# Kernel optimization log

Hardware: AMD Instinct MI355X
Metric: run time of the kernel (lower is better)

Reference implementation:

```python
import jax, jax.numpy as jnp
import numpy as np

B, T, D = 1024, 20, 50          # batch sessions, seq len (hardcoded 20), emb dim (hardcoded 50)
S1S2 = 50 * 20                  # sample1 * sample2 friend nodes (GAT src)
DEG = 50                        # avg in-degree per dst node
E = B * DEG
NUM_USERS, NUM_ITEMS = 100000, 50000


def _lstm(x, W_ih, W_hh, b_ih, b_hh):
    """PyTorch-style LSTM (gate order i,f,g,o). x: [N,T,D] -> hs: [T,N,D]."""
    N = x.shape[0]
    h0 = jnp.zeros((N, x.shape[-1]), x.dtype)
    def step(carry, xt):
        h, c = carry
        gates = xt @ W_ih.T + h @ W_hh.T + b_ih + b_hh
        i, f, g, o = jnp.split(gates, 4, axis=-1)
        c = jax.nn.sigmoid(f) * c + jax.nn.sigmoid(i) * jnp.tanh(g)
        h = jax.nn.sigmoid(o) * jnp.tanh(c)
        return (h, c), h
    (_, _), hs = jax.lax.scan(step, (h0, h0), jnp.swapaxes(x, 0, 1))
    return hs


def _gat(feat_src, feat_dst, edge_src, edge_dst, fc_W, fc_b):
    """u_dot_v -> edge_softmax (per dst) -> u_mul_e_sum -> relu(fc)."""
    n_dst = feat_dst.shape[0]
    src_e = feat_src[edge_src]                           # [E, D] gather
    score = jnp.sum(src_e * feat_dst[edge_dst], axis=-1) # [E] u_dot_v
    m = jax.ops.segment_max(score, edge_dst, num_segments=n_dst)
    ex = jnp.exp(score - m[edge_dst])
    den = jax.ops.segment_sum(ex, edge_dst, num_segments=n_dst)
    w = ex / den[edge_dst]                               # edge_softmax
    agg = jax.ops.segment_sum(w[:, None] * src_e, edge_dst, num_segments=n_dst)
    return jax.nn.relu(agg @ fc_W.T + fc_b)


def setup_inputs() -> dict:
    key = jax.random.key(0)
    ks = jax.random.split(key, 16)
    input_session = jax.random.randint(ks[0], (B, T), 0, NUM_ITEMS, dtype=jnp.int32)
    support_nodes_layer1 = jax.random.randint(ks[1], (S1S2,), 0, NUM_USERS, dtype=jnp.int32)
    support_sessions_layer1 = jax.random.randint(ks[2], (S1S2, T), 0, NUM_ITEMS, dtype=jnp.int32)
    edge_src = jax.random.randint(ks[3], (E,), 0, S1S2, dtype=jnp.int32)
    edge_dst = jnp.repeat(jnp.arange(B, dtype=jnp.int32), DEG)  # every dst has DEG edges
    s = 0.05
    user_emb = jax.random.normal(ks[4], (NUM_USERS, D), jnp.float32) * s
    item_emb = (jax.random.normal(ks[5], (NUM_ITEMS, D), jnp.float32) * s).at[0].set(0.0)  # padding_idx=0
    W_ih = jax.random.normal(ks[6], (4 * D, D), jnp.float32) * s
    W_hh = jax.random.normal(ks[7], (4 * D, D), jnp.float32) * s
    b_ih = jax.random.normal(ks[8], (4 * D,), jnp.float32) * s
    b_hh = jax.random.normal(ks[9], (4 * D,), jnp.float32) * s
    W1 = jax.random.normal(ks[10], (D, 2 * D), jnp.float32) * s
    fc_W = jax.random.normal(ks[11], (D, D), jnp.float32) * s
    fc_b = jax.random.normal(ks[12], (D,), jnp.float32) * s
    W2 = jax.random.normal(ks[13], (D, 3 * D), jnp.float32) * s
    return {"input_session": input_session, "support_nodes_layer1": support_nodes_layer1,
            "support_sessions_layer1": support_sessions_layer1, "edge_src": edge_src,
            "edge_dst": edge_dst, "user_emb": user_emb, "item_emb": item_emb,
            "W_ih": W_ih, "W_hh": W_hh, "b_ih": b_ih, "b_hh": b_hh,
            "W1": W1, "fc_W": fc_W, "fc_b": fc_b, "W2": W2}


def reference(input_session, support_nodes_layer1, support_sessions_layer1, edge_src, edge_dst,
              user_emb, item_emb, W_ih, W_hh, b_ih, b_hh, W1, fc_W, fc_b, W2):
    # current-user short-term: LSTM over session item embeddings, take last hidden
    output = _lstm(item_emb[input_session], W_ih, W_hh, b_ih, b_hh)[-1]        # [B, D]
    # friends long-term (user emb) + short-term (LSTM over friend sessions, step 0 as in source)
    long_term1 = user_emb[support_nodes_layer1]                                 # [S1S2, D]
    short_term1 = _lstm(item_emb[support_sessions_layer1], W_ih, W_hh, b_ih, b_hh)[0]  # [S1S2, D]
    ls1 = jax.nn.relu(jnp.concatenate([long_term1, short_term1], axis=-1) @ W1.T)      # [S1S2, D]
    # GAT: gather -> per-dst edge softmax -> scatter weighted sum
    gat_out = _gat(ls1, output, edge_src, edge_dst, fc_W, fc_b)                 # [B, D]
    feat = jnp.concatenate([output, gat_out], axis=-1)                          # [B, 2D]
    sr = jnp.concatenate([output, feat], axis=-1) @ W2.T                        # [B, D]
    logits = sr @ item_emb[1:].T                                                # [B, NUM_ITEMS-1]
    return logits
```

## Files before the change

kernel.cpp:

```cpp
#include <hip/hip_runtime.h>
#include <math.h>

#define D 50
#define T 20
#define BATCH 1024
#define S1S2 1000
#define DEG 50
#define NITEMS 50000
#define NLOGITS 49999
#define KPAD 64
#define NIPAD 50048
#define LROW 520

using bf16x8 = __attribute__((ext_vector_type(8))) __bf16;
using f32x4  = __attribute__((ext_vector_type(4))) float;

__device__ __forceinline__ float sigf(float x) { return 1.0f / (1.0f + expf(-x)); }

__device__ __forceinline__ unsigned short f2bf(float f) {
    unsigned u = __builtin_bit_cast(unsigned, f);
    u = (u + 0x7FFFu + ((u >> 16) & 1u)) >> 16;
    return (unsigned short)u;
}

__global__ __launch_bounds__(256) void lstm_main_kernel(
    const int* __restrict__ sess,
    const float* __restrict__ item_emb,
    const float* __restrict__ W_ih,
    const float* __restrict__ W_hh,
    const float* __restrict__ b_ih,
    const float* __restrict__ b_hh,
    float* __restrict__ out_h)
{
    const int b = blockIdx.x;
    const int t = threadIdx.x;
    __shared__ float x_s[D];
    __shared__ float h_s[D];
    __shared__ float g_s[4 * D];
    __shared__ int idx_s[T];

    if (t < T) idx_s[t] = sess[b * T + t];

    float wih[D], whh[D];
    float bias = 0.f;
    if (t < 4 * D) {
        #pragma unroll
        for (int k = 0; k < D; ++k) {
            wih[k] = W_ih[t * D + k];
            whh[k] = W_hh[t * D + k];
        }
        bias = b_ih[t] + b_hh[t];
    }
    float c = 0.f;
    if (t < D) h_s[t] = 0.f;
    __syncthreads();

    for (int step = 0; step < T; ++step) {
        if (t < D) x_s[t] = item_emb[(size_t)idx_s[step] * D + t];
        __syncthreads();
        if (t < 4 * D) {
            float g = bias;
            #pragma unroll
            for (int k = 0; k < D; ++k)
                g += wih[k] * x_s[k] + whh[k] * h_s[k];
            g_s[t] = g;
        }
        __syncthreads();
        if (t < D) {
            float ig = sigf(g_s[t]);
            float fg = sigf(g_s[D + t]);
            float gg = tanhf(g_s[2 * D + t]);
            float og = sigf(g_s[3 * D + t]);
            c = fg * c + ig * gg;
            h_s[t] = og * tanhf(c);
        }
        __syncthreads();
    }
    if (t < D) out_h[b * D + t] = h_s[t];
}

__global__ __launch_bounds__(256) void friends_kernel(
    const int* __restrict__ nodes,
    const int* __restrict__ fsess,
    const float* __restrict__ user_emb,
    const float* __restrict__ item_emb,
    const float* __restrict__ W_ih,
    const float* __restrict__ W_hh,
    const float* __restrict__ b_ih,
    const float* __restrict__ b_hh,
    const float* __restrict__ W1,
    float* __restrict__ ls1)
{
    const int s = blockIdx.x;
    const int t = threadIdx.x;
    __shared__ float x_s[D];
    __shared__ float h_s[D];
    __shared__ float g_s[4 * D];

    if (t < D) x_s[t] = item_emb[(size_t)fsess[s * T] * D + t];
    __syncthreads();
    if (t < 4 * D) {
        float g = b_ih[t] + b_hh[t];
        #pragma unroll
        for (int k = 0; k < D; ++k) g += W_ih[t * D + k] * x_s[k];
        g_s[t] = g;
    }
    __syncthreads();
    if (t < D) {
        float ig = sigf(g_s[t]);
        float gg = tanhf(g_s[2 * D + t]);
        float og = sigf(g_s[3 * D + t]);
        float c1 = ig * gg;
        h_s[t] = og * tanhf(c1);
    }
    __syncthreads();
    if (t < D) {
        const int node = nodes[s];
        const float* ue = user_emb + (size_t)node * D;
        const float* w1r = W1 + t * 2 * D;
        float acc = 0.f;
        #pragma unroll
        for (int k = 0; k < D; ++k) acc += ue[k] * w1r[k];
        #pragma unroll
        for (int k = 0; k < D; ++k) acc += h_s[k] * w1r[D + k];
        ls1[s * D + t] = fmaxf(acc, 0.f);
    }
}

__global__ __launch_bounds__(64) void gat_sr_kernel(
    const float* __restrict__ out_h,
    const float* __restrict__ ls1,
    const int* __restrict__ edge_src,
    const float* __restrict__ fc_W,
    const float* __restrict__ fc_b,
    const float* __restrict__ W2,
    unsigned* __restrict__ sr_u)
{
    const int b = blockIdx.x;
    const int l = threadIdx.x;
    __shared__ float q[D];
    __shared__ int srcs[DEG];
    __shared__ float w_s[DEG];
    __shared__ float a_s[D];
    __shared__ float g_s[D];
    __shared__ float srow_s[KPAD];

    srow_s[l] = 0.f;
    if (l < D) q[l] = out_h[b * D + l];
    if (l < DEG) srcs[l] = edge_src[b * DEG + l];
    __syncthreads();

    float sc = -INFINITY;
    if (l < DEG) {
        const float* row = ls1 + (size_t)srcs[l] * D;
        float s = 0.f;
        #pragma unroll
        for (int k = 0; k < D; ++k) s += row[k] * q[k];
        sc = s;
    }
    float m = sc;
    #pragma unroll
    for (int off = 32; off; off >>= 1) m = fmaxf(m, __shfl_xor(m, off));
    float ex = (l < DEG) ? expf(sc - m) : 0.f;
    float den = ex;
    #pragma unroll
    for (int off = 32; off; off >>= 1) den += __shfl_xor(den, off);
    if (l < DEG) w_s[l] = ex / den;
    __syncthreads();

    if (l < D) {
        float a = 0.f;
        #pragma unroll
        for (int j = 0; j < DEG; ++j) a += w_s[j] * ls1[(size_t)srcs[j] * D + l];
        a_s[l] = a;
    }
    __syncthreads();
    if (l < D) {
        float g = fc_b[l];
        #pragma unroll
        for (int k = 0; k < D; ++k) g += a_s[k] * fc_W[l * D + k];
        g_s[l] = fmaxf(g, 0.f);
    }
    __syncthreads();
    if (l < D) {
        const float* w2r = W2 + l * 3 * D;
        float v = 0.f;
        #pragma unroll
        for (int k = 0; k < D; ++k) v += q[k] * (w2r[k] + w2r[D + k]);
        #pragma unroll
        for (int k = 0; k < D; ++k) v += g_s[k] * w2r[2 * D + k];
        srow_s[l] = v;
    }
    __syncthreads();
    if (l < KPAD / 2) {
        unsigned u = (unsigned)f2bf(srow_s[2 * l]) |
                     ((unsigned)f2bf(srow_s[2 * l + 1]) << 16);
        sr_u[b * (KPAD / 2) + l] = u;
    }
}

__global__ __launch_bounds__(256) void item_prep_kernel(
    const float* __restrict__ item_emb,
    unsigned* __restrict__ item_u)
{
    const int idx = blockIdx.x * 256 + threadIdx.x;
    if (idx >= NIPAD * (KPAD / 2)) return;
    const int r = idx >> 5, c2 = idx & 31;
    const int c0 = c2 * 2, c1 = c0 + 1;
    float f0 = 0.f, f1 = 0.f;
    if (r < NLOGITS) {
        const float* row = item_emb + (size_t)(1 + r) * D;
        if (c0 < D) f0 = row[c0];
        if (c1 < D) f1 = row[c1];
    }
    item_u[idx] = (unsigned)f2bf(f0) | ((unsigned)f2bf(f1) << 16);
}

__global__ __launch_bounds__(256) void logits_mfma_kernel(
    const unsigned short* __restrict__ sr_bf,
    const unsigned short* __restrict__ item_bf,
    float* __restrict__ out)
{
    const int t = threadIdx.x;
    const int lane = t & 63;
    const int wave = t >> 6;
    const int r16 = lane & 15;
    const int g   = lane >> 4;
    const int b0 = blockIdx.x * 16;
    const int ibase = blockIdx.y * 512;
    const int i0w = ibase + wave * 128;

    __shared__ float ls[16 * LROW];

    const unsigned short* bp = sr_bf + (size_t)(b0 + r16) * KPAD + g * 8;
    bf16x8 bv0 = *(const bf16x8*)(bp);
    bf16x8 bv1 = *(const bf16x8*)(bp + 32);

    #pragma unroll
    for (int m = 0; m < 8; ++m) {
        int irow = i0w + m * 16 + r16;
        const unsigned short* ap =
            item_bf + (size_t)(irow < NIPAD ? irow : NIPAD - 1) * KPAD + g * 8;
        bf16x8 av0 = *(const bf16x8*)(ap);
        bf16x8 av1 = *(const bf16x8*)(ap + 32);
        f32x4 acc = {0.f, 0.f, 0.f, 0.f};
        acc = __builtin_amdgcn_mfma_f32_16x16x32_bf16(av0, bv0, acc, 0, 0, 0);
        acc = __builtin_amdgcn_mfma_f32_16x16x32_bf16(av1, bv1, acc, 0, 0, 0);
        *(f32x4*)&ls[r16 * LROW + wave * 128 + m * 16 + g * 4] = acc;
    }
    __syncthreads();

    #pragma unroll
    for (int pass = 0; pass < 4; ++pass) {
        const int row = wave * 4 + pass;
        float* orow = out + (size_t)(b0 + row) * NLOGITS + ibase;
        #pragma unroll
        for (int it2 = 0; it2 < 2; ++it2) {
            const int c = lane * 4 + it2 * 256;
            const int i = ibase + c;
            f32x4 v = *(const f32x4*)&ls[row * LROW + c];
            if (i + 3 < NLOGITS) {
                *(float4*)(orow + c) = make_float4(v[0], v[1], v[2], v[3]);
            } else {
                #pragma unroll
                for (int r = 0; r < 4; ++r)
                    if (i + r < NLOGITS) orow[c + r] = v[r];
            }
        }
    }
}

extern "C" void kernel_launch(void* const* d_in, const int* in_sizes, int n_in,
                              void* d_out, int out_size, void* d_ws, size_t ws_size,
                              hipStream_t stream) {
    const int*   sess      = (const int*)d_in[0];
    const int*   nodes     = (const int*)d_in[1];
    const int*   fsess     = (const int*)d_in[2];
    const int*   edge_src  = (const int*)d_in[3];
    const float* user_emb  = (const float*)d_in[5];
    const float* item_emb  = (const float*)d_in[6];
    const float* W_ih      = (const float*)d_in[7];
    const float* W_hh      = (const float*)d_in[8];
    const float* b_ih      = (const float*)d_in[9];
    const float* b_hh      = (const float*)d_in[10];
    const float* W1        = (const float*)d_in[11];
    const float* fc_W      = (const float*)d_in[12];
    const float* fc_b      = (const float*)d_in[13];
    const float* W2        = (const float*)d_in[14];
    float* out = (float*)d_out;

    char* ws = (char*)d_ws;
    float*    out_h  = (float*)(ws);
    float*    ls1    = (float*)(ws + 204800);
    unsigned* sr_u   = (unsigned*)(ws + 404800);
    unsigned* item_u = (unsigned*)(ws + 535872);

    hipLaunchKernelGGL(item_prep_kernel,
                       dim3((NIPAD * (KPAD / 2) + 255) / 256), dim3(256), 0, stream,
                       item_emb, item_u);
    hipLaunchKernelGGL(lstm_main_kernel, dim3(BATCH), dim3(256), 0, stream,
                       sess, item_emb, W_ih, W_hh, b_ih, b_hh, out_h);
    hipLaunchKernelGGL(friends_kernel, dim3(S1S2), dim3(256), 0, stream,
                       nodes, fsess, user_emb, item_emb, W_ih, W_hh, b_ih, b_hh, W1, ls1);
    hipLaunchKernelGGL(gat_sr_kernel, dim3(BATCH), dim3(64), 0, stream,
                       out_h, ls1, edge_src, fc_W, fc_b, W2, sr_u);
    hipLaunchKernelGGL(logits_mfma_kernel,
                       dim3(BATCH / 16, (NLOGITS + 511) / 512), dim3(256), 0, stream,
                       (const unsigned short*)sr_u, (const unsigned short*)item_u, out);
}
```

Before: 125.6 us.

## Fuse LSTM, friends and item-prep kernels; prefetch LSTM input; remap logits grid

Merges the main LSTM, the friends LSTM/W1 projection and the bf16 item-embedding prep into one heterogeneous launch, so the three independent stages can run concurrently and two launch gaps disappear. Inside the main LSTM, the next step's embedding row is loaded while the current gates are computed, which removes one barrier per step. The logits kernel moves to a 1D grid with a permuted chunk order, and padded blocks exit early. In exchange the fused kernel carries register pressure from the LSTM weights into every block, which may reduce occupancy for the lightweight prep blocks.

```diff
diff --git a/kernel.cpp b/kernel.cpp
--- a/kernel.cpp
+++ b/kernel.cpp
@@ -11,6 +11,9 @@
 #define KPAD 64
 #define NIPAD 50048
 #define LROW 520
+#define CHUNKS 98
+#define CHUNKS_PAD 104
+#define PREP_BLKS ((NIPAD * (KPAD / 2) + 255) / 256)
 
 using bf16x8 = __attribute__((ext_vector_type(8))) __bf16;
 using f32x4  = __attribute__((ext_vector_type(4))) float;
@@ -23,63 +26,8 @@
     return (unsigned short)u;
 }
 
-__global__ __launch_bounds__(256) void lstm_main_kernel(
+__global__ __launch_bounds__(256) void fused_front_kernel(
     const int* __restrict__ sess,
-    const float* __restrict__ item_emb,
-    const float* __restrict__ W_ih,
-    const float* __restrict__ W_hh,
-    const float* __restrict__ b_ih,
-    const float* __restrict__ b_hh,
-    float* __restrict__ out_h)
-{
-    const int b = blockIdx.x;
-    const int t = threadIdx.x;
-    __shared__ float x_s[D];
-    __shared__ float h_s[D];
-    __shared__ float g_s[4 * D];
-    __shared__ int idx_s[T];
-
-    if (t < T) idx_s[t] = sess[b * T + t];
-
-    float wih[D], whh[D];
-    float bias = 0.f;
-    if (t < 4 * D) {
-        #pragma unroll
-        for (int k = 0; k < D; ++k) {
-            wih[k] = W_ih[t * D + k];
-            whh[k] = W_hh[t * D + k];
-        }
-        bias = b_ih[t] + b_hh[t];
-    }
-    float c = 0.f;
-    if (t < D) h_s[t] = 0.f;
-    __syncthreads();
-
-    for (int step = 0; step < T; ++step) {
-        if (t < D) x_s[t] = item_emb[(size_t)idx_s[step] * D + t];
-        __syncthreads();
-        if (t < 4 * D) {
-            float g = bias;
-            #pragma unroll
-            for (int k = 0; k < D; ++k)
-                g += wih[k] * x_s[k] + whh[k] * h_s[k];
-            g_s[t] = g;
-        }
-        __syncthreads();
-        if (t < D) {
-            float ig = sigf(g_s[t]);
-            float fg = sigf(g_s[D + t]);
-            float gg = tanhf(g_s[2 * D + t]);
-            float og = sigf(g_s[3 * D + t]);
-            c = fg * c + ig * gg;
-            h_s[t] = og * tanhf(c);
-        }
-        __syncthreads();
-    }
-    if (t < D) out_h[b * D + t] = h_s[t];
-}
-
-__global__ __launch_bounds__(256) void friends_kernel(
     const int* __restrict__ nodes,
     const int* __restrict__ fsess,
     const float* __restrict__ user_emb,
@@ -89,41 +37,108 @@
     const float* __restrict__ b_ih,
     const float* __restrict__ b_hh,
     const float* __restrict__ W1,
-    float* __restrict__ ls1)
+    float* __restrict__ out_h,
+    float* __restrict__ ls1,
+    unsigned* __restrict__ item_u)
 {
-    const int s = blockIdx.x;
+    const int blk = blockIdx.x;
     const int t = threadIdx.x;
-    __shared__ float x_s[D];
-    __shared__ float h_s[D];
-    __shared__ float g_s[4 * D];
-
-    if (t < D) x_s[t] = item_emb[(size_t)fsess[s * T] * D + t];
-    __syncthreads();
-    if (t < 4 * D) {
-        float g = b_ih[t] + b_hh[t];
-        #pragma unroll
-        for (int k = 0; k < D; ++k) g += W_ih[t * D + k] * x_s[k];
-        g_s[t] = g;
-    }
-    __syncthreads();
-    if (t < D) {
-        float ig = sigf(g_s[t]);
-        float gg = tanhf(g_s[2 * D + t]);
-        float og = sigf(g_s[3 * D + t]);
-        float c1 = ig * gg;
-        h_s[t] = og * tanhf(c1);
-    }
-    __syncthreads();
-    if (t < D) {
-        const int node = nodes[s];
-        const float* ue = user_emb + (size_t)node * D;
-        const float* w1r = W1 + t * 2 * D;
-        float acc = 0.f;
-        #pragma unroll
-        for (int k = 0; k < D; ++k) acc += ue[k] * w1r[k];
-        #pragma unroll
-        for (int k = 0; k < D; ++k) acc += h_s[k] * w1r[D + k];
-        ls1[s * D + t] = fmaxf(acc, 0.f);
+
+    if (blk < BATCH) {
+        const int b = blk;
+        __shared__ float x_s[D];
+        __shared__ float h_s[D];
+        __shared__ float g_s[4 * D];
+        __shared__ int idx_s[T];
+
+        if (t < T) idx_s[t] = sess[b * T + t];
+
+        float wih[D], whh[D];
+        float bias = 0.f;
+        if (t < 4 * D) {
+            #pragma unroll
+            for (int k = 0; k < D; ++k) {
+                wih[k] = W_ih[t * D + k];
+                whh[k] = W_hh[t * D + k];
+            }
+            bias = b_ih[t] + b_hh[t];
+        }
+        float c = 0.f;
+        if (t < D) h_s[t] = 0.f;
+        __syncthreads();
+        if (t < D) x_s[t] = item_emb[(size_t)idx_s[0] * D + t];
+        __syncthreads();
+
+        for (int step = 0; step < T; ++step) {
+            float xn = 0.f;
+            if (t < D && step + 1 < T)
+                xn = item_emb[(size_t)idx_s[step + 1] * D + t];
+            if (t < 4 * D) {
+                float g = bias;
+                #pragma unroll
+                for (int k = 0; k < D; ++k)
+                    g += wih[k] * x_s[k] + whh[k] * h_s[k];
+                g_s[t] = g;
+            }
+            __syncthreads();
+            if (t < D) {
+                float ig = sigf(g_s[t]);
+                float fg = sigf(g_s[D + t]);
+                float gg = tanhf(g_s[2 * D + t]);
+                float og = sigf(g_s[3 * D + t]);
+                c = fg * c + ig * gg;
+                h_s[t] = og * tanhf(c);
+                if (step + 1 < T) x_s[t] = xn;
+            }
+            __syncthreads();
+        }
+        if (t < D) out_h[b * D + t] = h_s[t];
+    } else if (blk < BATCH + S1S2) {
+        const int s = blk - BATCH;
+        __shared__ float fx_s[D];
+        __shared__ float fh_s[D];
+        __shared__ float fg_s[4 * D];
+
+        if (t < D) fx_s[t] = item_emb[(size_t)fsess[s * T] * D + t];
+        __syncthreads();
+        if (t < 4 * D) {
+            float g = b_ih[t] + b_hh[t];
+            #pragma unroll
+            for (int k = 0; k < D; ++k) g += W_ih[t * D + k] * fx_s[k];
+            fg_s[t] = g;
+        }
+        __syncthreads();
+        if (t < D) {
+            float ig = sigf(fg_s[t]);
+            float gg = tanhf(fg_s[2 * D + t]);
+            float og = sigf(fg_s[3 * D + t]);
+            float c1 = ig * gg;
+            fh_s[t] = og * tanhf(c1);
+        }
+        __syncthreads();
+        if (t < D) {
+            const int node = nodes[s];
+            const float* ue = user_emb + (size_t)node * D;
+            const float* w1r = W1 + t * 2 * D;
+            float acc = 0.f;
+            #pragma unroll
+            for (int k = 0; k < D; ++k) acc += ue[k] * w1r[k];
+            #pragma unroll
+            for (int k = 0; k < D; ++k) acc += fh_s[k] * w1r[D + k];
+            ls1[s * D + t] = fmaxf(acc, 0.f);
+        }
+    } else {
+        const int idx = (blk - BATCH - S1S2) * 256 + t;
+        if (idx >= NIPAD * (KPAD / 2)) return;
+        const int r = idx >> 5, c2 = idx & 31;
+        const int c0 = c2 * 2, c1 = c0 + 1;
+        float f0 = 0.f, f1 = 0.f;
+        if (r < NLOGITS) {
+            const float* row = item_emb + (size_t)(1 + r) * D;
+            if (c0 < D) f0 = row[c0];
+            if (c1 < D) f1 = row[c1];
+        }
+        item_u[idx] = (unsigned)f2bf(f0) | ((unsigned)f2bf(f1) << 16);
     }
 }
 
@@ -199,35 +214,24 @@
     }
 }
 
-__global__ __launch_bounds__(256) void item_prep_kernel(
-    const float* __restrict__ item_emb,
-    unsigned* __restrict__ item_u)
-{
-    const int idx = blockIdx.x * 256 + threadIdx.x;
-    if (idx >= NIPAD * (KPAD / 2)) return;
-    const int r = idx >> 5, c2 = idx & 31;
-    const int c0 = c2 * 2, c1 = c0 + 1;
-    float f0 = 0.f, f1 = 0.f;
-    if (r < NLOGITS) {
-        const float* row = item_emb + (size_t)(1 + r) * D;
-        if (c0 < D) f0 = row[c0];
-        if (c1 < D) f1 = row[c1];
-    }
-    item_u[idx] = (unsigned)f2bf(f0) | ((unsigned)f2bf(f1) << 16);
-}
-
 __global__ __launch_bounds__(256) void logits_mfma_kernel(
     const unsigned short* __restrict__ sr_bf,
     const unsigned short* __restrict__ item_bf,
     float* __restrict__ out)
 {
+    const int n = blockIdx.x;
+    const int slab = n / CHUNKS_PAD;
+    const int j = n - slab * CHUNKS_PAD;
+    const int chunk = (j & 7) * 13 + (j >> 3);
+    if (chunk >= CHUNKS) return;
+
     const int t = threadIdx.x;
     const int lane = t & 63;
     const int wave = t >> 6;
     const int r16 = lane & 15;
     const int g   = lane >> 4;
-    const int b0 = blockIdx.x * 16;
-    const int ibase = blockIdx.y * 512;
+    const int b0 = slab * 16;
+    const int ibase = chunk * 512;
     const int i0w = ibase + wave * 128;
 
     __shared__ float ls[16 * LROW];
@@ -295,16 +299,13 @@
     unsigned* sr_u   = (unsigned*)(ws + 404800);
     unsigned* item_u = (unsigned*)(ws + 535872);
 
-    hipLaunchKernelGGL(item_prep_kernel,
-                       dim3((NIPAD * (KPAD / 2) + 255) / 256), dim3(256), 0, stream,
-                       item_emb, item_u);
-    hipLaunchKernelGGL(lstm_main_kernel, dim3(BATCH), dim3(256), 0, stream,
-                       sess, item_emb, W_ih, W_hh, b_ih, b_hh, out_h);
-    hipLaunchKernelGGL(friends_kernel, dim3(S1S2), dim3(256), 0, stream,
-                       nodes, fsess, user_emb, item_emb, W_ih, W_hh, b_ih, b_hh, W1, ls1);
+    hipLaunchKernelGGL(fused_front_kernel,
+                       dim3(BATCH + S1S2 + PREP_BLKS), dim3(256), 0, stream,
+                       sess, nodes, fsess, user_emb, item_emb,
+                       W_ih, W_hh, b_ih, b_hh, W1, out_h, ls1, item_u);
     hipLaunchKernelGGL(gat_sr_kernel, dim3(BATCH), dim3(64), 0, stream,
                        out_h, ls1, edge_src, fc_W, fc_b, W2, sr_u);
     hipLaunchKernelGGL(logits_mfma_kernel,
-                       dim3(BATCH / 16, (NLOGITS + 511) / 512), dim3(256), 0, stream,
+                       dim3((BATCH / 16) * CHUNKS_PAD), dim3(256), 0, stream,
                        (const unsigned short*)sr_u, (const unsigned short*)item_u, out);
 }
```

Measured after the change: 111.9 us. -10.9%, faster.
